# Optimization experiments

Measured on AMD Instinct MI355X. Metric: run time of the kernel, lower is better.

## Reference

```python
import jax, jax.numpy as jnp
import numpy as np

TAU = 1.0
F_BIAS = 1.0
EPS = 1e-5


def chunk_ln(x, g, b, n):
    # layernorm applied independently over n chunks of the last dim
    B, D = x.shape
    d = D // n
    xr = x.reshape(B, n, d)
    mu = xr.mean(axis=2, keepdims=True)
    var = xr.var(axis=2, keepdims=True)
    xr = (xr - mu) / jnp.sqrt(var + EPS)
    return xr.reshape(B, D) * g + b


def setup_inputs() -> dict:
    key = jax.random.key(0)
    ks = jax.random.split(key, 16)
    B, X, H, M, K = 256, 512, 1024, 128, 64
    inp = {
        "x": jax.random.normal(ks[0], (B, X), jnp.float32),
        "c": jax.random.normal(ks[1], (B, H), jnp.float32),
        "hmem": jax.random.normal(ks[2], (B, M, H), jnp.float32),
        "u_t": jax.random.uniform(ks[3], (B, M), jnp.float32),
        "prev_read_location": jnp.zeros((B, M), jnp.float32),
        "gumbel_u": jax.random.uniform(ks[4], (B, M), jnp.float32, minval=1e-6, maxval=1.0),
        "keys": jax.random.normal(ks[5], (M, K), jnp.float32) * 0.1,
        "vec_a": jax.random.normal(ks[6], (H // 4, 1), jnp.float32) * 0.1,
        "fc_w": jax.random.normal(ks[7], (X + 2 * H + K + M, H // 4), jnp.float32) * (1.0 / np.sqrt(X + 2 * H + K + M)),
        "fc_b": jnp.zeros((H // 4,), jnp.float32),
        "W_full": jax.random.normal(ks[8], (X + 2 * H, 5 * H), jnp.float32) * (1.0 / np.sqrt(X + 2 * H)),
        "bias": jnp.zeros((5 * H,), jnp.float32),
        "W_full1": jax.random.normal(ks[9], (X + 2 * H, 2 * H), jnp.float32) * (1.0 / np.sqrt(X + 2 * H)),
        "bias1": jnp.zeros((2 * H,), jnp.float32),
        "ln1_g": jnp.ones((5 * H,), jnp.float32), "ln1_b": jnp.zeros((5 * H,), jnp.float32),
        "ln2_g": jnp.ones((H,), jnp.float32), "ln2_b": jnp.zeros((H,), jnp.float32),
        "ln3_g": jnp.ones((2 * H,), jnp.float32), "ln3_b": jnp.zeros((2 * H,), jnp.float32),
        "ln4_g": jnp.ones((M,), jnp.float32), "ln4_b": jnp.zeros((M,), jnp.float32),
    }
    return inp


def reference(x, c, hmem, u_t, prev_read_location, gumbel_u,
              keys, vec_a, fc_w, fc_b, W_full, bias, W_full1, bias1,
              ln1_g, ln1_b, ln2_g, ln2_b, ln3_g, ln3_b, ln4_g, ln4_b):
    B, X = x.shape
    H = c.shape[1]
    M = keys.shape[0]
    # --- content-addressed read head ---
    xc = jnp.concatenate([x, c], axis=1)                      # [B, X+H]
    u_norm = u_t / jnp.maximum(jnp.linalg.norm(u_t, axis=1, keepdims=True), 1e-12)
    feat = jnp.concatenate([
        jnp.broadcast_to(xc[:, None, :], (B, M, xc.shape[1])),
        jnp.broadcast_to(keys[None, :, :], (B, M, keys.shape[1])),
        hmem,
        jnp.broadcast_to(u_norm[:, None, :], (B, M, M)),
    ], axis=2)                                                # [B, M, X+2H+K+M]
    hfeat = jnp.tanh(feat @ fc_w + fc_b)                      # [B, M, H//4]
    score = jnp.einsum('bmk,k->bm', hfeat, vec_a[:, 0])       # [B, M]
    score = score - prev_read_location * 100.0
    score = chunk_ln(score, ln4_g, ln4_b, 1)
    # --- gumbel-softmax hard read (straight-through) ---
    gumbel = -jnp.log(1e-20 - jnp.log(1e-20 + gumbel_u))
    y = jax.nn.softmax((score + gumbel) * TAU, axis=1)
    ymax = jnp.max(y, axis=1, keepdims=True)
    hard = (y == ymax).astype(y.dtype)
    h_read_index = jax.lax.stop_gradient(hard - y) + y        # one-hot fwd, soft bwd
    h_entry = jnp.einsum('bm,bmh->bh', h_read_index, hmem)    # [B, H]
    # --- gated LSTM-style cell ---
    concat0 = jnp.concatenate([x, c, h_entry], axis=1)        # [B, X+2H]
    g1 = jax.nn.sigmoid(chunk_ln(concat0 @ W_full1 + bias1, ln3_g, ln3_b, 2))
    gate = jnp.concatenate([jnp.ones_like(x), g1], axis=1)
    concat0 = concat0 * gate
    z = chunk_ln(concat0 @ W_full + bias, ln1_g, ln1_b, 5)
    i, j, f, o, om = jnp.split(z, 5, axis=1)
    new_c = c * jax.nn.sigmoid(f + F_BIAS) + jax.nn.sigmoid(i) * jnp.tanh(j)
    new_c = chunk_ln(new_c, ln2_g, ln2_b, 1)
    new_h = jnp.tanh(new_c) * jax.nn.sigmoid(o)
    r = jnp.tanh(h_entry) * jax.nn.sigmoid(om)
    new_r = jnp.concatenate([new_h, r], axis=1)               # [B, 2H]
    return new_r
```

## Files before the change

### kernel.cpp

```cpp
#include <hip/hip_runtime.h>
#include <cstdint>
#include <cstddef>

typedef unsigned short u16;
typedef float floatx4 __attribute__((ext_vector_type(4)));
typedef __bf16 bf16x8 __attribute__((ext_vector_type(8)));
typedef unsigned short u16x8 __attribute__((ext_vector_type(8)));
typedef unsigned short u16x4 __attribute__((ext_vector_type(4)));

__device__ __forceinline__ u16 f2bf(float f) {
  unsigned u = __float_as_uint(f);
  unsigned r = u + 0x7FFFu + ((u >> 16) & 1u);
  return (u16)(r >> 16);
}
__device__ __forceinline__ float bf2f(u16 h) {
  return __uint_as_float(((unsigned)h) << 16);
}
__device__ __forceinline__ void gl_lds16(const void* g, void* l) {
  __builtin_amdgcn_global_load_lds(
      (const __attribute__((address_space(1))) unsigned int*)g,
      (__attribute__((address_space(3))) unsigned int*)l, 16, 0, 0);
}
__device__ __forceinline__ float wsum(float v) {
#pragma unroll
  for (int m = 32; m > 0; m >>= 1) v += __shfl_xor(v, m, 64);
  return v;
}
__device__ __forceinline__ float wmaxr(float v) {
#pragma unroll
  for (int m = 32; m > 0; m >>= 1) v = fmaxf(v, __shfl_xor(v, m, 64));
  return v;
}
template <int NW>
__device__ __forceinline__ float bsum(float v, float* sh) {
  int lane = threadIdx.x & 63, wid = threadIdx.x >> 6;
  v = wsum(v);
  __syncthreads();
  if (lane == 0) sh[wid] = v;
  __syncthreads();
  float t = 0.f;
#pragma unroll
  for (int i = 0; i < NW; ++i) t += sh[i];
  return t;
}
template <int NW>
__device__ __forceinline__ float bmaxr(float v, float* sh) {
  int lane = threadIdx.x & 63, wid = threadIdx.x >> 6;
  v = wmaxr(v);
  __syncthreads();
  if (lane == 0) sh[wid] = v;
  __syncthreads();
  float t = sh[0];
#pragma unroll
  for (int i = 1; i < NW; ++i) t = fmaxf(t, sh[i]);
  return t;
}
__device__ __forceinline__ float sigm(float x) { return 1.0f / (1.0f + expf(-x)); }

__global__ __launch_bounds__(256) void k_prep(
    const float* __restrict__ fcw, const float* __restrict__ keys,
    const float* __restrict__ ut, const float* __restrict__ fcb,
    u16* __restrict__ W3H, u16* __restrict__ W3L,
    float* __restrict__ A2, float* __restrict__ UN) {
  __shared__ float kr[64];
  __shared__ float shs[4];
  int blk = blockIdx.x, t = threadIdx.x;
  if (blk < 128) {
    int ks = blk >> 2, q = blk & 3;
    int slot = q ^ ((t >> 1) & 3);
    u16x8 vh, vl;
#pragma unroll
    for (int e = 0; e < 8; ++e) {
      float f = fcw[(size_t)(1600 + ks * 32 + q * 8 + e) * 256 + t];
      u16 h = f2bf(f);
      vh[e] = h;
      vl[e] = f2bf(f - bf2f(h));
    }
    *(u16x8*)&W3H[(size_t)ks * 8192 + t * 32 + slot * 8] = vh;
    *(u16x8*)&W3L[(size_t)ks * 8192 + t * 32 + slot * 8] = vl;
  } else if (blk < 256) {
    int m = blk - 128;
    if (t < 64) kr[t] = keys[m * 64 + t];
    __syncthreads();
    float acc = fcb[t];
#pragma unroll 8
    for (int j = 0; j < 64; ++j)
      acc = fmaf(kr[j], fcw[(size_t)(1536 + j) * 256 + t], acc);
    A2[m * 256 + t] = acc;
  } else {
    int b = blk - 256;
    float v = (t < 128) ? ut[b * 128 + t] : 0.f;
    float s = bsum<4>(v * v, shs);
    float dnm = fmaxf(sqrtf(s), 1e-12f);
    if (t < 128) UN[b * 128 + t] = v / dnm;
  }
}

__global__ __launch_bounds__(256) void k_a1(
    const float* __restrict__ x, const float* __restrict__ c,
    const float* __restrict__ un, const float* __restrict__ fcw,
    float* __restrict__ A1) {
  __shared__ float sh[512];
  int kc = blockIdx.x % 26;
  int bg = blockIdx.x / 26;
  int t = threadIdx.x;
  int g0 = kc * 64;
  int row_base = (g0 < 1536) ? g0 : g0 + 1088;
#pragma unroll
  for (int p = 0; p < 2; ++p) {
    int idx = p * 256 + t;
    int bl = idx >> 6, j = idx & 63;
    int b = bg * 8 + bl;
    int g = g0 + j;
    float v;
    if (g < 512) v = x[b * 512 + g];
    else if (g < 1536) v = c[b * 1024 + (g - 512)];
    else v = un[b * 128 + (g - 1536)];
    sh[idx] = v;
  }
  __syncthreads();
  float acc[8];
#pragma unroll
  for (int i = 0; i < 8; ++i) acc[i] = 0.f;
#pragma unroll 4
  for (int j = 0; j < 64; ++j) {
    float wv = fcw[(size_t)(row_base + j) * 256 + t];
#pragma unroll
    for (int bl = 0; bl < 8; ++bl)
      acc[bl] = fmaf(sh[bl * 64 + j], wv, acc[bl]);
  }
#pragma unroll
  for (int bl = 0; bl < 8; ++bl)
    atomicAdd(&A1[(bg * 8 + bl) * 256 + t], acc[bl]);
}

__global__ __launch_bounds__(512, 2) void k2_score(
    const float* __restrict__ hmem, const u16* __restrict__ Bhp,
    const u16* __restrict__ Blp, const float* __restrict__ A1,
    const float* __restrict__ A2, const float* __restrict__ va,
    float* __restrict__ sp) {
  __shared__ __align__(16) u16 Ah[2][4096];
  __shared__ __align__(16) u16 Al[2][4096];
  __shared__ __align__(16) u16 Bh[2][8192];
  __shared__ __align__(16) u16 Bl[2][8192];
  const int b = blockIdx.x;
  const int t = threadIdx.x;
  const int lane = t & 63, w = t >> 6;
  const int q = lane >> 4, r16 = lane & 15;
  const int rh = w >> 2, cq = w & 3;
  const int slot = q ^ ((r16 >> 1) & 3);

  floatx4 acc[4][4];
#pragma unroll
  for (int i = 0; i < 4; ++i)
#pragma unroll
    for (int j = 0; j < 4; ++j) acc[i][j] = (floatx4){0.f, 0.f, 0.f, 0.f};

  const int m_st = t >> 2, qh = t & 3;
  const int wslot = qh ^ ((m_st >> 1) & 3);
  const int aw_idx = m_st * 32 + wslot * 8;
  const float* aptr = hmem + ((size_t)(b * 128 + m_st)) * 1024 + qh * 8;

  int aoff[4], boff[4];
#pragma unroll
  for (int i = 0; i < 4; ++i) {
    int row = rh * 64 + i * 16 + r16;
    aoff[i] = row * 32 + slot * 8;
  }
#pragma unroll
  for (int ct = 0; ct < 4; ++ct) {
    int col = cq * 64 + ct * 16 + r16;
    boff[ct] = col * 32 + slot * 8;
  }

#pragma unroll
  for (int i = 0; i < 2; ++i) {
    int L = (w * 2 + i) * 1024 + lane * 16;
    gl_lds16((const char*)Bhp + L, (char*)&Bh[0][0] + L);
    gl_lds16((const char*)Blp + L, (char*)&Bl[0][0] + L);
  }
  float pv[8];
#pragma unroll
  for (int i = 0; i < 8; ++i) pv[i] = aptr[i];
  {
    u16x8 hh, ll;
#pragma unroll
    for (int i = 0; i < 8; ++i) {
      u16 h = f2bf(pv[i]);
      hh[i] = h;
      ll[i] = f2bf(pv[i] - bf2f(h));
    }
    *(u16x8*)&Ah[0][aw_idx] = hh;
    *(u16x8*)&Al[0][aw_idx] = ll;
  }
#pragma unroll
  for (int i = 0; i < 8; ++i) pv[i] = aptr[32 + i];

  for (int ks = 0; ks < 32; ++ks) {
    const int cur = ks & 1, nxt = cur ^ 1;
    __syncthreads();
    if (ks < 31) {
#pragma unroll
      for (int i = 0; i < 2; ++i) {
        int L = (w * 2 + i) * 1024 + lane * 16;
        gl_lds16((const char*)Bhp + (size_t)(ks + 1) * 16384 + L, (char*)&Bh[nxt][0] + L);
        gl_lds16((const char*)Blp + (size_t)(ks + 1) * 16384 + L, (char*)&Bl[nxt][0] + L);
      }
      u16x8 hh, ll;
#pragma unroll
      for (int i = 0; i < 8; ++i) {
        u16 h = f2bf(pv[i]);
        hh[i] = h;
        ll[i] = f2bf(pv[i] - bf2f(h));
      }
      *(u16x8*)&Ah[nxt][aw_idx] = hh;
      *(u16x8*)&Al[nxt][aw_idx] = ll;
      if (ks < 30) {
        const float* np = aptr + (ks + 2) * 32;
#pragma unroll
        for (int i = 0; i < 8; ++i) pv[i] = np[i];
      }
    }
    bf16x8 ah[4], al[4];
#pragma unroll
    for (int i = 0; i < 4; ++i) {
      ah[i] = __builtin_bit_cast(bf16x8, *(const u16x8*)&Ah[cur][aoff[i]]);
      al[i] = __builtin_bit_cast(bf16x8, *(const u16x8*)&Al[cur][aoff[i]]);
    }
#pragma unroll
    for (int ct = 0; ct < 4; ++ct) {
      bf16x8 bh = __builtin_bit_cast(bf16x8, *(const u16x8*)&Bh[cur][boff[ct]]);
      bf16x8 bl = __builtin_bit_cast(bf16x8, *(const u16x8*)&Bl[cur][boff[ct]]);
#pragma unroll
      for (int i = 0; i < 4; ++i) {
        acc[i][ct] = __builtin_amdgcn_mfma_f32_16x16x32_bf16(ah[i], bh, acc[i][ct], 0, 0, 0);
        acc[i][ct] = __builtin_amdgcn_mfma_f32_16x16x32_bf16(ah[i], bl, acc[i][ct], 0, 0, 0);
        acc[i][ct] = __builtin_amdgcn_mfma_f32_16x16x32_bf16(al[i], bh, acc[i][ct], 0, 0, 0);
      }
    }
  }
  float rs[4][4];
#pragma unroll
  for (int i = 0; i < 4; ++i)
#pragma unroll
    for (int r = 0; r < 4; ++r) rs[i][r] = 0.f;
#pragma unroll
  for (int ct = 0; ct < 4; ++ct) {
    int col = cq * 64 + ct * 16 + r16;
    float a1v = A1[b * 256 + col];
    float vav = va[col];
#pragma unroll
    for (int i = 0; i < 4; ++i) {
      int row0 = rh * 64 + i * 16 + q * 4;
#pragma unroll
      for (int r = 0; r < 4; ++r) {
        float pre = acc[i][ct][r] + a1v + A2[(row0 + r) * 256 + col];
        rs[i][r] += tanhf(pre) * vav;
      }
    }
  }
#pragma unroll
  for (int mask = 1; mask <= 8; mask <<= 1)
#pragma unroll
    for (int i = 0; i < 4; ++i)
#pragma unroll
      for (int r = 0; r < 4; ++r) rs[i][r] += __shfl_xor(rs[i][r], mask, 64);
  if (r16 == 0) {
#pragma unroll
    for (int i = 0; i < 4; ++i)
#pragma unroll
      for (int r = 0; r < 4; ++r) {
        int row = rh * 64 + i * 16 + q * 4 + r;
        sp[cq * 32768 + b * 128 + row] = rs[i][r];
      }
  }
}

__global__ __launch_bounds__(128) void k3_softmax(
    const float* __restrict__ sp, const float* __restrict__ prev,
    const float* __restrict__ gu, const float* __restrict__ g4,
    const float* __restrict__ b4, float* __restrict__ wgt) {
  __shared__ float shs[2];
  int b = blockIdx.x, m = threadIdx.x;
  int bm = b * 128 + m;
  float s = sp[bm] + sp[32768 + bm] + sp[65536 + bm] + sp[98304 + bm];
  s -= prev[bm] * 100.0f;
  float mu = bsum<2>(s, shs) * (1.0f / 128.0f);
  float d = s - mu;
  float var = bsum<2>(d * d, shs) * (1.0f / 128.0f);
  float sn = d / sqrtf(var + 1e-5f) * g4[m] + b4[m];
  float gv = -logf(1e-20f - logf(1e-20f + gu[bm]));
  float z = (sn + gv) * 1.0f;
  float zm = bmaxr<2>(z, shs);
  float e = expf(z - zm);
  float Zs = bsum<2>(e, shs);
  float y = e / Zs;
  float ym = bmaxr<2>(y, shs);
  float hard = (y == ym) ? 1.0f : 0.0f;
  wgt[bm] = (hard - y) + y;
}

__global__ __launch_bounds__(256) void k4_gather(
    const float* __restrict__ wgt, const float* __restrict__ hmem,
    const float* __restrict__ x, const float* __restrict__ c,
    float* __restrict__ he, u16* __restrict__ ab1) {
  __shared__ float wsw[128];
  int b = blockIdx.x, t = threadIdx.x;
  if (t < 128) wsw[t] = wgt[b * 128 + t];
  __syncthreads();
  float4 a;
  a.x = a.y = a.z = a.w = 0.f;
  for (int mm = 0; mm < 128; ++mm) {
    float wm = wsw[mm];
    if (wm != 0.0f) {
      float4 v = ((const float4*)(hmem + ((size_t)(b * 128 + mm)) * 1024))[t];
      a.x = fmaf(wm, v.x, a.x);
      a.y = fmaf(wm, v.y, a.y);
      a.z = fmaf(wm, v.z, a.z);
      a.w = fmaf(wm, v.w, a.w);
    }
  }
  ((float4*)(he + (size_t)b * 1024))[t] = a;
  const int sx = ((b >> 1) & 3) << 3;
  u16* row = ab1 + (size_t)b * 2560;
  if (t < 128) {
    float4 xv = ((const float4*)(x + (size_t)b * 512))[t];
    u16x4 o = {f2bf(xv.x), f2bf(xv.y), f2bf(xv.z), f2bf(xv.w)};
    *(u16x4*)&row[(t * 4) ^ sx] = o;
  }
  {
    float4 cv = ((const float4*)(c + (size_t)b * 1024))[t];
    u16x4 o = {f2bf(cv.x), f2bf(cv.y), f2bf(cv.z), f2bf(cv.w)};
    *(u16x4*)&row[(512 + t * 4) ^ sx] = o;
  }
  {
    u16x4 o = {f2bf(a.x), f2bf(a.y), f2bf(a.z), f2bf(a.w)};
    *(u16x4*)&row[(1536 + t * 4) ^ sx] = o;
  }
}

__global__ __launch_bounds__(256) void gemm_cell(
    const u16* __restrict__ Abf, const float* __restrict__ W,
    float* __restrict__ Z, int N, int nblk, int nsteps) {
  __shared__ __align__(16) u16 Asm[256 * 32];
  __shared__ __align__(16) float Bf[32 * 64];
  __shared__ __align__(16) u16 Bsm[64 * 40];
  int cb = blockIdx.x % nblk;
  int kc = blockIdx.x / nblk;
  int t = threadIdx.x, lane = t & 63, w = t >> 6;
  int q = lane >> 4, r16 = lane & 15;
  const int axor = ((r16 >> 1) & 3) << 3;
  floatx4 acc[4][4];
#pragma unroll
  for (int i = 0; i < 4; ++i)
#pragma unroll
    for (int j = 0; j < 4; ++j) acc[i][j] = (floatx4){0.f, 0.f, 0.f, 0.f};
  int k0 = kc * nsteps * 32;
  for (int ks = 0; ks < nsteps; ++ks) {
    int k = k0 + ks * 32;
#pragma unroll
    for (int i = 0; i < 4; ++i) {
      int L = (w * 4 + i) * 1024 + lane * 16;
      int row = L >> 6, off = L & 63;
      gl_lds16((const char*)Abf + (size_t)row * 5120 + k * 2 + off, (char*)Asm + L);
    }
#pragma unroll
    for (int i = 0; i < 2; ++i) {
      int L = (w * 2 + i) * 1024 + lane * 16;
      int kr = L >> 8, off = L & 255;
      gl_lds16((const char*)W + ((size_t)(k + kr) * N + cb * 64) * 4 + off, (char*)Bf + L);
    }
    __syncthreads();
    {
      int cc = t & 63, p = t >> 6;
      u16x8 hh;
#pragma unroll
      for (int i2 = 0; i2 < 8; ++i2) hh[i2] = f2bf(Bf[(p * 8 + i2) * 64 + cc]);
      *(u16x8*)&Bsm[cc * 40 + p * 8] = hh;
    }
    __syncthreads();
    bf16x8 af[4];
#pragma unroll
    for (int i = 0; i < 4; ++i) {
      int row = w * 64 + i * 16 + r16;
      af[i] = __builtin_bit_cast(bf16x8, *(const u16x8*)&Asm[(row * 32 + q * 8) ^ axor]);
    }
#pragma unroll
    for (int ct = 0; ct < 4; ++ct) {
      int col = ct * 16 + r16;
      bf16x8 bb = __builtin_bit_cast(bf16x8, *(const u16x8*)&Bsm[col * 40 + q * 8]);
#pragma unroll
      for (int i = 0; i < 4; ++i)
        acc[i][ct] = __builtin_amdgcn_mfma_f32_16x16x32_bf16(af[i], bb, acc[i][ct], 0, 0, 0);
    }
    __syncthreads();
  }
#pragma unroll
  for (int ct = 0; ct < 4; ++ct)
#pragma unroll
    for (int i = 0; i < 4; ++i)
#pragma unroll
      for (int r = 0; r < 4; ++r) {
        int col = cb * 64 + ct * 16 + r16;
        int row = w * 64 + i * 16 + q * 4 + r;
        atomicAdd(&Z[(size_t)row * N + col], acc[i][ct][r]);
      }
}

__global__ __launch_bounds__(256) void k5b(
    const float* __restrict__ Z1, const float* __restrict__ bias1,
    const float* __restrict__ x, const float* __restrict__ c,
    const float* __restrict__ he, const float* __restrict__ g3,
    const float* __restrict__ b3, u16* __restrict__ ab2) {
  __shared__ float shs[4];
  int b = blockIdx.x, t = threadIdx.x;
  const float4* zp = (const float4*)(Z1 + (size_t)b * 2048);
  const float4* bp = (const float4*)bias1;
  float4 z0v = zp[t], z1v = zp[256 + t];
  float4 q0 = bp[t], q1 = bp[256 + t];
  float za[4] = {z0v.x + q0.x, z0v.y + q0.y, z0v.z + q0.z, z0v.w + q0.w};
  float zb[4] = {z1v.x + q1.x, z1v.y + q1.y, z1v.z + q1.z, z1v.w + q1.w};
  float g1a[4], g1b[4];
  {
    float s = za[0] + za[1] + za[2] + za[3];
    float mu = bsum<4>(s, shs) * (1.0f / 1024.0f);
    float ss = 0.f;
#pragma unroll
    for (int i = 0; i < 4; ++i) { float d = za[i] - mu; ss += d * d; }
    float var = bsum<4>(ss, shs) * (1.0f / 1024.0f);
    float r = sqrtf(var + 1e-5f);
    float4 gv = ((const float4*)g3)[t];
    float4 bv = ((const float4*)b3)[t];
    g1a[0] = sigm((za[0] - mu) / r * gv.x + bv.x);
    g1a[1] = sigm((za[1] - mu) / r * gv.y + bv.y);
    g1a[2] = sigm((za[2] - mu) / r * gv.z + bv.z);
    g1a[3] = sigm((za[3] - mu) / r * gv.w + bv.w);
  }
  {
    float s = zb[0] + zb[1] + zb[2] + zb[3];
    float mu = bsum<4>(s, shs) * (1.0f / 1024.0f);
    float ss = 0.f;
#pragma unroll
    for (int i = 0; i < 4; ++i) { float d = zb[i] - mu; ss += d * d; }
    float var = bsum<4>(ss, shs) * (1.0f / 1024.0f);
    float r = sqrtf(var + 1e-5f);
    float4 gv = ((const float4*)g3)[256 + t];
    float4 bv = ((const float4*)b3)[256 + t];
    g1b[0] = sigm((zb[0] - mu) / r * gv.x + bv.x);
    g1b[1] = sigm((zb[1] - mu) / r * gv.y + bv.y);
    g1b[2] = sigm((zb[2] - mu) / r * gv.z + bv.z);
    g1b[3] = sigm((zb[3] - mu) / r * gv.w + bv.w);
  }
  const int sx = ((b >> 1) & 3) << 3;
  u16* row = ab2 + (size_t)b * 2560;
  if (t < 128) {
    float4 xv = ((const float4*)(x + (size_t)b * 512))[t];
    u16x4 o = {f2bf(xv.x), f2bf(xv.y), f2bf(xv.z), f2bf(xv.w)};
    *(u16x4*)&row[(t * 4) ^ sx] = o;
  }
  {
    float4 cv = ((const float4*)(c + (size_t)b * 1024))[t];
    u16x4 o = {f2bf(cv.x * g1a[0]), f2bf(cv.y * g1a[1]), f2bf(cv.z * g1a[2]), f2bf(cv.w * g1a[3])};
    *(u16x4*)&row[(512 + t * 4) ^ sx] = o;
  }
  {
    float4 hv = ((const float4*)(he + (size_t)b * 1024))[t];
    u16x4 o = {f2bf(hv.x * g1b[0]), f2bf(hv.y * g1b[1]), f2bf(hv.z * g1b[2]), f2bf(hv.w * g1b[3])};
    *(u16x4*)&row[(1536 + t * 4) ^ sx] = o;
  }
}

__global__ __launch_bounds__(256) void k5d(
    const float* __restrict__ Z2, const float* __restrict__ bias,
    const float* __restrict__ c, const float* __restrict__ he,
    const float* __restrict__ g1, const float* __restrict__ b1,
    const float* __restrict__ g2, const float* __restrict__ b2,
    float* __restrict__ out) {
  __shared__ float shs[4];
  int b = blockIdx.x, t = threadIdx.x;
  const float4* zp = (const float4*)(Z2 + (size_t)b * 5120);
  const float4* bp = (const float4*)bias;
  float z[5][4];
#pragma unroll
  for (int ci = 0; ci < 5; ++ci) {
    float4 v = zp[ci * 256 + t];
    float4 bb = bp[ci * 256 + t];
    z[ci][0] = v.x + bb.x; z[ci][1] = v.y + bb.y;
    z[ci][2] = v.z + bb.z; z[ci][3] = v.w + bb.w;
  }
#pragma unroll
  for (int ci = 0; ci < 5; ++ci) {
    float s = z[ci][0] + z[ci][1] + z[ci][2] + z[ci][3];
    float mu = bsum<4>(s, shs) * (1.0f / 1024.0f);
    float ss = 0.f;
#pragma unroll
    for (int i = 0; i < 4; ++i) { float d = z[ci][i] - mu; ss += d * d; }
    float var = bsum<4>(ss, shs) * (1.0f / 1024.0f);
    float r = sqrtf(var + 1e-5f);
    float4 gv = ((const float4*)g1)[ci * 256 + t];
    float4 bv = ((const float4*)b1)[ci * 256 + t];
    z[ci][0] = (z[ci][0] - mu) / r * gv.x + bv.x;
    z[ci][1] = (z[ci][1] - mu) / r * gv.y + bv.y;
    z[ci][2] = (z[ci][2] - mu) / r * gv.z + bv.z;
    z[ci][3] = (z[ci][3] - mu) / r * gv.w + bv.w;
  }
  float4 cv = ((const float4*)(c + (size_t)b * 1024))[t];
  float cvv[4] = {cv.x, cv.y, cv.z, cv.w};
  float nc[4];
#pragma unroll
  for (int i = 0; i < 4; ++i)
    nc[i] = cvv[i] * sigm(z[2][i] + 1.0f) + sigm(z[0][i]) * tanhf(z[1][i]);
  float s = nc[0] + nc[1] + nc[2] + nc[3];
  float mu = bsum<4>(s, shs) * (1.0f / 1024.0f);
  float ss = 0.f;
#pragma unroll
  for (int i = 0; i < 4; ++i) { float d = nc[i] - mu; ss += d * d; }
  float var = bsum<4>(ss, shs) * (1.0f / 1024.0f);
  float r2 = sqrtf(var + 1e-5f);
  float4 g2v = ((const float4*)g2)[t];
  float4 b2v = ((const float4*)b2)[t];
  float g2a[4] = {g2v.x, g2v.y, g2v.z, g2v.w};
  float b2a[4] = {b2v.x, b2v.y, b2v.z, b2v.w};
  float4 hv = ((const float4*)(he + (size_t)b * 1024))[t];
  float hva[4] = {hv.x, hv.y, hv.z, hv.w};
  float4 o1, o2;
  float nh[4], rr[4];
#pragma unroll
  for (int i = 0; i < 4; ++i) {
    float ncn = (nc[i] - mu) / r2 * g2a[i] + b2a[i];
    nh[i] = tanhf(ncn) * sigm(z[3][i]);
    rr[i] = tanhf(hva[i]) * sigm(z[4][i]);
  }
  o1.x = nh[0]; o1.y = nh[1]; o1.z = nh[2]; o1.w = nh[3];
  o2.x = rr[0]; o2.y = rr[1]; o2.z = rr[2]; o2.w = rr[3];
  ((float4*)(out + (size_t)b * 2048))[t] = o1;
  ((float4*)(out + (size_t)b * 2048 + 1024))[t] = o2;
}

extern "C" void kernel_launch(void* const* d_in, const int* in_sizes, int n_in,
                              void* d_out, int out_size, void* d_ws, size_t ws_size,
                              hipStream_t stream) {
  const float* x = (const float*)d_in[0];
  const float* c = (const float*)d_in[1];
  const float* hmem = (const float*)d_in[2];
  const float* ut = (const float*)d_in[3];
  const float* prev = (const float*)d_in[4];
  const float* gu = (const float*)d_in[5];
  const float* keys = (const float*)d_in[6];
  const float* veca = (const float*)d_in[7];
  const float* fcw = (const float*)d_in[8];
  const float* fcb = (const float*)d_in[9];
  const float* Wf = (const float*)d_in[10];
  const float* bias = (const float*)d_in[11];
  const float* Wf1 = (const float*)d_in[12];
  const float* bias1 = (const float*)d_in[13];
  const float* ln1g = (const float*)d_in[14];
  const float* ln1b = (const float*)d_in[15];
  const float* ln2g = (const float*)d_in[16];
  const float* ln2b = (const float*)d_in[17];
  const float* ln3g = (const float*)d_in[18];
  const float* ln3b = (const float*)d_in[19];
  const float* ln4g = (const float*)d_in[20];
  const float* ln4b = (const float*)d_in[21];

  char* ws = (char*)d_ws;
  float* UN = (float*)(ws + 0);
  float* A2 = (float*)(ws + 131072);
  float* A1 = (float*)(ws + 262144);
  u16* W3H = (u16*)(ws + 524288);
  u16* W3L = (u16*)(ws + 1048576);
  float* SP = (float*)(ws + 1572864);
  float* WGT = (float*)(ws + 2097152);
  float* HE = (float*)(ws + 2228224);
  u16* AB1 = (u16*)(ws + 3276800);
  u16* AB2 = (u16*)(ws + 4587520);
  float* Z1 = (float*)(ws + 5898240);
  float* Z2 = (float*)(ws + 7995392);

  hipMemsetAsync(A1, 0, (size_t)256 * 256 * 4, stream);
  hipMemsetAsync(Z1, 0, (size_t)256 * 2048 * 4, stream);
  hipMemsetAsync(Z2, 0, (size_t)256 * 5120 * 4, stream);
  k_prep<<<512, 256, 0, stream>>>(fcw, keys, ut, fcb, W3H, W3L, A2, UN);
  k_a1<<<832, 256, 0, stream>>>(x, c, UN, fcw, A1);
  k2_score<<<256, 512, 0, stream>>>(hmem, W3H, W3L, A1, A2, veca, SP);
  k3_softmax<<<256, 128, 0, stream>>>(SP, prev, gu, ln4g, ln4b, WGT);
  k4_gather<<<256, 256, 0, stream>>>(WGT, hmem, x, c, HE, AB1);
  gemm_cell<<<32 * 8, 256, 0, stream>>>(AB1, Wf1, Z1, 2048, 32, 10);
  k5b<<<256, 256, 0, stream>>>(Z1, bias1, x, c, HE, ln3g, ln3b, AB2);
  gemm_cell<<<80 * 4, 256, 0, stream>>>(AB2, Wf, Z2, 5120, 80, 20);
  k5d<<<256, 256, 0, stream>>>(Z2, bias, c, HE, ln1g, ln1b, ln2g, ln2b, (float*)d_out);
}
```

Before: 441.4 us.

## Split score kernel per half-batch, fuse softmax with gather, replace atomics with split-K partials

The score kernel now runs two 256-thread blocks per batch row, each covering 64 memory slots, which doubles the grid for more parallelism. The cost is that each block loads the full B tile again. The softmax and gather kernels are merged into one, removing a launch and the weight round-trip through global memory. The cell GEMMs now write per-K-chunk partial sums to separate buffers instead of using atomicAdd, which drops the two large memsets and the atomics. The follow-up kernels sum those partials, at the price of more global memory traffic.

```diff
diff --git a/kernel.cpp b/kernel.cpp
--- a/kernel.cpp
+++ b/kernel.cpp
@@ -134,20 +134,20 @@
     atomicAdd(&A1[(bg * 8 + bl) * 256 + t], acc[bl]);
 }
 
-__global__ __launch_bounds__(512, 2) void k2_score(
+__global__ __launch_bounds__(256, 2) void k2_score(
     const float* __restrict__ hmem, const u16* __restrict__ Bhp,
     const u16* __restrict__ Blp, const float* __restrict__ A1,
     const float* __restrict__ A2, const float* __restrict__ va,
     float* __restrict__ sp) {
-  __shared__ __align__(16) u16 Ah[2][4096];
-  __shared__ __align__(16) u16 Al[2][4096];
+  __shared__ __align__(16) u16 Ah[2][2048];
+  __shared__ __align__(16) u16 Al[2][2048];
   __shared__ __align__(16) u16 Bh[2][8192];
   __shared__ __align__(16) u16 Bl[2][8192];
-  const int b = blockIdx.x;
+  const int b = blockIdx.x >> 1, hf = blockIdx.x & 1;
   const int t = threadIdx.x;
   const int lane = t & 63, w = t >> 6;
   const int q = lane >> 4, r16 = lane & 15;
-  const int rh = w >> 2, cq = w & 3;
+  const int cq = w;
   const int slot = q ^ ((r16 >> 1) & 3);
 
   floatx4 acc[4][4];
@@ -159,23 +159,17 @@
   const int m_st = t >> 2, qh = t & 3;
   const int wslot = qh ^ ((m_st >> 1) & 3);
   const int aw_idx = m_st * 32 + wslot * 8;
-  const float* aptr = hmem + ((size_t)(b * 128 + m_st)) * 1024 + qh * 8;
+  const float* aptr = hmem + ((size_t)(b * 128 + hf * 64 + m_st)) * 1024 + qh * 8;
 
   int aoff[4], boff[4];
 #pragma unroll
+  for (int i = 0; i < 4; ++i) aoff[i] = (i * 16 + r16) * 32 + slot * 8;
+#pragma unroll
+  for (int ct = 0; ct < 4; ++ct) boff[ct] = (cq * 64 + ct * 16 + r16) * 32 + slot * 8;
+
+#pragma unroll
   for (int i = 0; i < 4; ++i) {
-    int row = rh * 64 + i * 16 + r16;
-    aoff[i] = row * 32 + slot * 8;
-  }
-#pragma unroll
-  for (int ct = 0; ct < 4; ++ct) {
-    int col = cq * 64 + ct * 16 + r16;
-    boff[ct] = col * 32 + slot * 8;
-  }
-
-#pragma unroll
-  for (int i = 0; i < 2; ++i) {
-    int L = (w * 2 + i) * 1024 + lane * 16;
+    int L = (w * 4 + i) * 1024 + lane * 16;
     gl_lds16((const char*)Bhp + L, (char*)&Bh[0][0] + L);
     gl_lds16((const char*)Blp + L, (char*)&Bl[0][0] + L);
   }
@@ -201,8 +195,8 @@
     __syncthreads();
     if (ks < 31) {
 #pragma unroll
-      for (int i = 0; i < 2; ++i) {
-        int L = (w * 2 + i) * 1024 + lane * 16;
+      for (int i = 0; i < 4; ++i) {
+        int L = (w * 4 + i) * 1024 + lane * 16;
         gl_lds16((const char*)Bhp + (size_t)(ks + 1) * 16384 + L, (char*)&Bh[nxt][0] + L);
         gl_lds16((const char*)Blp + (size_t)(ks + 1) * 16384 + L, (char*)&Bl[nxt][0] + L);
       }
@@ -251,10 +245,10 @@
     float vav = va[col];
 #pragma unroll
     for (int i = 0; i < 4; ++i) {
-      int row0 = rh * 64 + i * 16 + q * 4;
+      int m0 = hf * 64 + i * 16 + q * 4;
 #pragma unroll
       for (int r = 0; r < 4; ++r) {
-        float pre = acc[i][ct][r] + a1v + A2[(row0 + r) * 256 + col];
+        float pre = acc[i][ct][r] + a1v + A2[(m0 + r) * 256 + col];
         rs[i][r] += tanhf(pre) * vav;
       }
     }
@@ -270,43 +264,45 @@
     for (int i = 0; i < 4; ++i)
 #pragma unroll
       for (int r = 0; r < 4; ++r) {
-        int row = rh * 64 + i * 16 + q * 4 + r;
+        int row = hf * 64 + i * 16 + q * 4 + r;
         sp[cq * 32768 + b * 128 + row] = rs[i][r];
       }
   }
 }
 
-__global__ __launch_bounds__(128) void k3_softmax(
+__global__ __launch_bounds__(256) void k34(
     const float* __restrict__ sp, const float* __restrict__ prev,
     const float* __restrict__ gu, const float* __restrict__ g4,
-    const float* __restrict__ b4, float* __restrict__ wgt) {
-  __shared__ float shs[2];
-  int b = blockIdx.x, m = threadIdx.x;
-  int bm = b * 128 + m;
-  float s = sp[bm] + sp[32768 + bm] + sp[65536 + bm] + sp[98304 + bm];
-  s -= prev[bm] * 100.0f;
-  float mu = bsum<2>(s, shs) * (1.0f / 128.0f);
-  float d = s - mu;
-  float var = bsum<2>(d * d, shs) * (1.0f / 128.0f);
-  float sn = d / sqrtf(var + 1e-5f) * g4[m] + b4[m];
-  float gv = -logf(1e-20f - logf(1e-20f + gu[bm]));
-  float z = (sn + gv) * 1.0f;
-  float zm = bmaxr<2>(z, shs);
-  float e = expf(z - zm);
-  float Zs = bsum<2>(e, shs);
-  float y = e / Zs;
-  float ym = bmaxr<2>(y, shs);
-  float hard = (y == ym) ? 1.0f : 0.0f;
-  wgt[bm] = (hard - y) + y;
-}
-
-__global__ __launch_bounds__(256) void k4_gather(
-    const float* __restrict__ wgt, const float* __restrict__ hmem,
+    const float* __restrict__ b4, const float* __restrict__ hmem,
     const float* __restrict__ x, const float* __restrict__ c,
     float* __restrict__ he, u16* __restrict__ ab1) {
   __shared__ float wsw[128];
+  __shared__ float shs[4];
   int b = blockIdx.x, t = threadIdx.x;
-  if (t < 128) wsw[t] = wgt[b * 128 + t];
+  bool act = (t < 128);
+  float s = 0.f;
+  if (act) {
+    int bm = b * 128 + t;
+    s = sp[bm] + sp[32768 + bm] + sp[65536 + bm] + sp[98304 + bm] - prev[bm] * 100.0f;
+  }
+  float mu = bsum<4>(s, shs) * (1.0f / 128.0f);
+  float d = act ? (s - mu) : 0.f;
+  float var = bsum<4>(d * d, shs) * (1.0f / 128.0f);
+  float z = -INFINITY;
+  if (act) {
+    float sn = d / sqrtf(var + 1e-5f) * g4[t] + b4[t];
+    float gv = -logf(1e-20f - logf(1e-20f + gu[b * 128 + t]));
+    z = sn + gv;
+  }
+  float zm = bmaxr<4>(z, shs);
+  float e = act ? expf(z - zm) : 0.f;
+  float Zs = bsum<4>(e, shs);
+  float y = e / Zs;
+  float ym = bmaxr<4>(y, shs);
+  if (act) {
+    float hard = (y == ym) ? 1.0f : 0.0f;
+    wsw[t] = (hard - y) + y;
+  }
   __syncthreads();
   float4 a;
   a.x = a.y = a.z = a.w = 0.f;
@@ -341,7 +337,7 @@
 
 __global__ __launch_bounds__(256) void gemm_cell(
     const u16* __restrict__ Abf, const float* __restrict__ W,
-    float* __restrict__ Z, int N, int nblk, int nsteps) {
+    float* __restrict__ Zp, int N, int nblk, int nsteps) {
   __shared__ __align__(16) u16 Asm[256 * 32];
   __shared__ __align__(16) float Bf[32 * 64];
   __shared__ __align__(16) u16 Bsm[64 * 40];
@@ -395,6 +391,7 @@
     }
     __syncthreads();
   }
+  float* dst = Zp + (size_t)kc * 256 * N;
 #pragma unroll
   for (int ct = 0; ct < 4; ++ct)
 #pragma unroll
@@ -403,23 +400,28 @@
       for (int r = 0; r < 4; ++r) {
         int col = cb * 64 + ct * 16 + r16;
         int row = w * 64 + i * 16 + q * 4 + r;
-        atomicAdd(&Z[(size_t)row * N + col], acc[i][ct][r]);
+        dst[(size_t)row * N + col] = acc[i][ct][r];
       }
 }
 
 __global__ __launch_bounds__(256) void k5b(
-    const float* __restrict__ Z1, const float* __restrict__ bias1,
+    const float* __restrict__ Z1p, const float* __restrict__ bias1,
     const float* __restrict__ x, const float* __restrict__ c,
     const float* __restrict__ he, const float* __restrict__ g3,
     const float* __restrict__ b3, u16* __restrict__ ab2) {
   __shared__ float shs[4];
   int b = blockIdx.x, t = threadIdx.x;
-  const float4* zp = (const float4*)(Z1 + (size_t)b * 2048);
   const float4* bp = (const float4*)bias1;
-  float4 z0v = zp[t], z1v = zp[256 + t];
   float4 q0 = bp[t], q1 = bp[256 + t];
-  float za[4] = {z0v.x + q0.x, z0v.y + q0.y, z0v.z + q0.z, z0v.w + q0.w};
-  float zb[4] = {z1v.x + q1.x, z1v.y + q1.y, z1v.z + q1.z, z1v.w + q1.w};
+  float za[4] = {q0.x, q0.y, q0.z, q0.w};
+  float zb[4] = {q1.x, q1.y, q1.z, q1.w};
+#pragma unroll
+  for (int kc = 0; kc < 8; ++kc) {
+    const float4* zp = (const float4*)(Z1p + (size_t)kc * 524288 + (size_t)b * 2048);
+    float4 v0 = zp[t], v1 = zp[256 + t];
+    za[0] += v0.x; za[1] += v0.y; za[2] += v0.z; za[3] += v0.w;
+    zb[0] += v1.x; zb[1] += v1.y; zb[2] += v1.z; zb[3] += v1.w;
+  }
   float g1a[4], g1b[4];
   {
     float s = za[0] + za[1] + za[2] + za[3];
@@ -471,22 +473,28 @@
 }
 
 __global__ __launch_bounds__(256) void k5d(
-    const float* __restrict__ Z2, const float* __restrict__ bias,
+    const float* __restrict__ Z2p, const float* __restrict__ bias,
     const float* __restrict__ c, const float* __restrict__ he,
     const float* __restrict__ g1, const float* __restrict__ b1,
     const float* __restrict__ g2, const float* __restrict__ b2,
     float* __restrict__ out) {
   __shared__ float shs[4];
   int b = blockIdx.x, t = threadIdx.x;
-  const float4* zp = (const float4*)(Z2 + (size_t)b * 5120);
   const float4* bp = (const float4*)bias;
   float z[5][4];
 #pragma unroll
   for (int ci = 0; ci < 5; ++ci) {
-    float4 v = zp[ci * 256 + t];
     float4 bb = bp[ci * 256 + t];
-    z[ci][0] = v.x + bb.x; z[ci][1] = v.y + bb.y;
-    z[ci][2] = v.z + bb.z; z[ci][3] = v.w + bb.w;
+    z[ci][0] = bb.x; z[ci][1] = bb.y; z[ci][2] = bb.z; z[ci][3] = bb.w;
+  }
+#pragma unroll
+  for (int kc = 0; kc < 4; ++kc) {
+    const float4* zp = (const float4*)(Z2p + (size_t)kc * 1310720 + (size_t)b * 5120);
+#pragma unroll
+    for (int ci = 0; ci < 5; ++ci) {
+      float4 v = zp[ci * 256 + t];
+      z[ci][0] += v.x; z[ci][1] += v.y; z[ci][2] += v.z; z[ci][3] += v.w;
+    }
   }
 #pragma unroll
   for (int ci = 0; ci < 5; ++ci) {
@@ -570,23 +578,19 @@
   u16* W3H = (u16*)(ws + 524288);
   u16* W3L = (u16*)(ws + 1048576);
   float* SP = (float*)(ws + 1572864);
-  float* WGT = (float*)(ws + 2097152);
-  float* HE = (float*)(ws + 2228224);
-  u16* AB1 = (u16*)(ws + 3276800);
-  u16* AB2 = (u16*)(ws + 4587520);
-  float* Z1 = (float*)(ws + 5898240);
-  float* Z2 = (float*)(ws + 7995392);
+  float* HE = (float*)(ws + 2097152);
+  u16* AB1 = (u16*)(ws + 3145728);
+  u16* AB2 = (u16*)(ws + 4456448);
+  float* Z1p = (float*)(ws + 5767168);
+  float* Z2p = (float*)(ws + 22544384);
 
   hipMemsetAsync(A1, 0, (size_t)256 * 256 * 4, stream);
-  hipMemsetAsync(Z1, 0, (size_t)256 * 2048 * 4, stream);
-  hipMemsetAsync(Z2, 0, (size_t)256 * 5120 * 4, stream);
   k_prep<<<512, 256, 0, stream>>>(fcw, keys, ut, fcb, W3H, W3L, A2, UN);
   k_a1<<<832, 256, 0, stream>>>(x, c, UN, fcw, A1);
-  k2_score<<<256, 512, 0, stream>>>(hmem, W3H, W3L, A1, A2, veca, SP);
-  k3_softmax<<<256, 128, 0, stream>>>(SP, prev, gu, ln4g, ln4b, WGT);
-  k4_gather<<<256, 256, 0, stream>>>(WGT, hmem, x, c, HE, AB1);
-  gemm_cell<<<32 * 8, 256, 0, stream>>>(AB1, Wf1, Z1, 2048, 32, 10);
-  k5b<<<256, 256, 0, stream>>>(Z1, bias1, x, c, HE, ln3g, ln3b, AB2);
-  gemm_cell<<<80 * 4, 256, 0, stream>>>(AB2, Wf, Z2, 5120, 80, 20);
-  k5d<<<256, 256, 0, stream>>>(Z2, bias, c, HE, ln1g, ln1b, ln2g, ln2b, (float*)d_out);
-}
+  k2_score<<<512, 256, 0, stream>>>(hmem, W3H, W3L, A1, A2, veca, SP);
+  k34<<<256, 256, 0, stream>>>(SP, prev, gu, ln4g, ln4b, hmem, x, c, HE, AB1);
+  gemm_cell<<<32 * 8, 256, 0, stream>>>(AB1, Wf1, Z1p, 2048, 32, 10);
+  k5b<<<256, 256, 0, stream>>>(Z1p, bias1, x, c, HE, ln3g, ln3b, AB2);
+  gemm_cell<<<80 * 4, 256, 0, stream>>>(AB2, Wf, Z2p, 5120, 80, 20);
+  k5d<<<256, 256, 0, stream>>>(Z2p, bias, c, HE, ln1g, ln1b, ln2g, ln2b, (float*)d_out);
+}
```

New measurement: 426.5 us. 3.4% less time.
